# Optimization experiments

Measured on AMD Instinct MI355X. Metric: run time of the kernel, lower is better.

The kernel has to match this reference:

```python
import jax, jax.numpy as jnp
import numpy as np

HEADS, DK, DV, STRIDE = 8, 32, 32, 2
EPS = 1e-5

def dwconv(x, w, b, stride):
    # depthwise 3x3, padding 1; w: [C,1,3,3]
    y = jax.lax.conv_general_dilated(
        x, w, (stride, stride), ((1, 1), (1, 1)),
        dimension_numbers=("NCHW", "OIHW", "NCHW"),
        feature_group_count=x.shape[1])
    return y + b[None, :, None, None]

def setup_inputs() -> dict:
    key = jax.random.key(0)
    ks = jax.random.split(key, 16)
    B_, C, H, W = 8, 256, 56, 56
    hd = HEADS * DK
    s = lambda k, shp: (jax.random.normal(k, shp, jnp.float32) * 0.02)
    return {
        "x": jax.random.normal(ks[0], (B_, C, H, W), jnp.float32),
        "Wk_dw": s(ks[1], (C, 1, 3, 3)), "bk_dw": jnp.zeros((C,), jnp.float32),
        "Wv_dw": s(ks[2], (C, 1, 3, 3)), "bv_dw": jnp.zeros((C,), jnp.float32),
        "Wq": s(ks[3], (hd, C)), "bq": jnp.zeros((hd,), jnp.float32),
        "Wk": s(ks[4], (hd, C)), "bk": jnp.zeros((hd,), jnp.float32),
        "Wv": s(ks[5], (HEADS * DV, C)), "bv": jnp.zeros((HEADS * DV,), jnp.float32),
        "Wo": s(ks[6], (C, HEADS * DV)), "bo": jnp.zeros((C,), jnp.float32),
        "Bbias": s(ks[7], (1, HEADS, H * W, (H // STRIDE) * (W // STRIDE))),
    }

def reference(x, Wk_dw, bk_dw, Wv_dw, bv_dw, Wq, bq, Wk, bk, Wv, bv, Wo, bo, Bbias):
    b, c, h, w = x.shape
    xr = x.reshape(b, c, h * w).transpose(0, 2, 1)  # [b, hw, c]
    # F.layer_norm with normalized_shape=(b, hw, c): single mean/var over ALL elements
    mu = jnp.mean(xr)
    var = jnp.mean((xr - mu) ** 2)
    xn = (xr - mu) * jax.lax.rsqrt(var + EPS)
    q = (xn @ Wq.T + bq).reshape(b, h * w, HEADS, DK).transpose(0, 2, 1, 3)  # [b,H,hw,dk]
    ki = dwconv(x, Wk_dw, bk_dw, STRIDE)
    kh, kw = ki.shape[2], ki.shape[3]
    kf = ki.reshape(b, c, kh * kw).transpose(0, 2, 1)
    k = (kf @ Wk.T + bk).reshape(b, kh * kw, HEADS, DK).transpose(0, 2, 1, 3)
    vi = dwconv(x, Wv_dw, bv_dw, STRIDE)
    vf = vi.reshape(b, c, kh * kw).transpose(0, 2, 1)
    v = (vf @ Wv.T + bv).reshape(b, kh * kw, HEADS, DV).transpose(0, 2, 1, 3)
    attn = jnp.einsum("bhid,bhjd->bhij", q, k) * (DK ** -0.5) + Bbias
    attn = jax.nn.softmax(attn, axis=-1)
    res = jnp.einsum("bhij,bhjd->bhid", attn, v).transpose(0, 2, 1, 3)
    res = res.reshape(b, h * w, HEADS * DV)
    out = (res @ Wo.T + bo).reshape(b, c, h, w)  # faithful to original .view (no transpose)
    return out + x
```

## Files before the change

### kernel.cpp

```cpp
#include <hip/hip_runtime.h>

typedef unsigned short u16;
typedef unsigned int   u32;
typedef __attribute__((ext_vector_type(8))) short short8;
typedef __attribute__((ext_vector_type(4))) float f32x4;
typedef __attribute__((ext_vector_type(4))) unsigned short us4;

#define MFMA16(a, b, c) __builtin_amdgcn_mfma_f32_16x16x32_bf16((a), (b), (c), 0, 0, 0)

static constexpr int B_ = 8;
static constexpr int HW = 3136;
static constexpr int KW = 784;
static constexpr int NELEM = B_ * 256 * HW;
static constexpr int NBB = 8 * HW * KW;

static constexpr size_t OFF_CNT = 4096;
static constexpr size_t OFF_W   = 8192;
static constexpr int AOFF_WQ = 0, AOFF_WK = 65536, AOFF_WV = 131072, AOFF_WO = 196608;
static constexpr int AOFF_WKDW = 262144, AOFF_WVDW = 264448;
static constexpr int AOFF_BKDW = 266752, AOFF_BVDW = 267008, AOFF_BQ = 267264;
static constexpr int AOFF_BK = 267520, AOFF_BV = 267776, AOFF_BO = 268032;
static constexpr size_t OFF_XT  = 557056;
static constexpr size_t SZ_XT   = (size_t)B_ * HW * 256 * 2;
static constexpr size_t SZ_KJ   = (size_t)B_ * KW * 256 * 2;
static constexpr size_t OFF_KIT = OFF_XT + SZ_XT;
static constexpr size_t OFF_VIT = OFF_KIT + SZ_KJ;
static constexpr size_t OFF_KI  = OFF_VIT + SZ_KJ;
static constexpr size_t OFF_VI  = OFF_KI + SZ_KJ;
static constexpr size_t OFF_Q   = OFF_VI + SZ_KJ;
static constexpr size_t OFF_O   = OFF_XT;
static constexpr size_t OFF_BB  = OFF_Q + SZ_XT;
static constexpr size_t SZ_BB   = (size_t)NBB * 2;

__device__ __forceinline__ float bf2f(u16 u) { return __uint_as_float(((u32)u) << 16); }
__device__ __forceinline__ u16 f2bf(float f) {
  u32 u = __float_as_uint(f);
  u32 r = u + 0x7FFFu + ((u >> 16) & 1u);
  return (u16)(r >> 16);
}
__device__ __forceinline__ u32 cvtpk(float lo, float hi) {
  u32 r;
  asm("v_cvt_pk_bf16_f32 %0, %1, %2" : "=v"(r) : "v"(lo), "v"(hi));
  return r;
}

__global__ __launch_bounds__(256) void detect_k(const u32* __restrict__ x, int* __restrict__ cnt) {
  int c = 0;
  for (int i = threadIdx.x; i < 4096; i += 256) {
    float v = __uint_as_float(x[i] << 16);
    if (fabsf(v) > 1e4f) c++;
  }
#pragma unroll
  for (int off = 32; off > 0; off >>= 1) c += __shfl_down(c, off);
  if ((threadIdx.x & 63) == 0) atomicAdd(cnt, c);
}

struct CvtArgs { const void* src[12]; int dstoff[12]; int n[12]; };
__global__ __launch_bounds__(256) void cvt_all_k(CvtArgs a, u16* __restrict__ arena,
                                                 const void* __restrict__ bsrc,
                                                 u16* __restrict__ bdst, int bias_blocks,
                                                 const int* __restrict__ cnt) {
  int f32m = (*cnt >= 64);
  int bid = blockIdx.x;
  if (bid < bias_blocks) {
    const int n4 = NBB / 4;
    if (f32m) {
      const float4* s = (const float4*)bsrc;
      us4* d = (us4*)bdst;
      for (int i = bid * 256 + threadIdx.x; i < n4; i += bias_blocks * 256) {
        float4 v = s[i];
        us4 o = {f2bf(v.x), f2bf(v.y), f2bf(v.z), f2bf(v.w)};
        d[i] = o;
      }
    } else {
      const uint2* s = (const uint2*)bsrc;
      uint2* d = (uint2*)bdst;
      for (int i = bid * 256 + threadIdx.x; i < n4; i += bias_blocks * 256) d[i] = s[i];
    }
    return;
  }
  int wb = bid - bias_blocks;
  int t = wb >> 2, sub = wb & 3;
  int n = a.n[t];
  u16* d = arena + a.dstoff[t];
  if (f32m) {
    const float* s = (const float*)a.src[t];
    for (int i = sub * 256 + threadIdx.x; i < n; i += 1024) d[i] = f2bf(s[i]);
  } else {
    const u16* s = (const u16*)a.src[t];
    for (int i = sub * 256 + threadIdx.x; i < n; i += 1024) d[i] = s[i];
  }
}

__global__ __launch_bounds__(256) void reduce_k(const void* __restrict__ x, double* __restrict__ acc,
                                                const int* __restrict__ cnt) {
  int f32m = (*cnt >= 64);
  float s = 0.f, ss = 0.f;
  if (f32m) {
    const float4* xv = (const float4*)x;
    const int n4 = NELEM / 4;
    for (int i = blockIdx.x * 256 + threadIdx.x; i < n4; i += gridDim.x * 256) {
      float4 u = xv[i];
      s += u.x + u.y + u.z + u.w;
      ss += u.x * u.x + u.y * u.y + u.z * u.z + u.w * u.w;
    }
  } else {
    const uint4* xv = (const uint4*)x;
    const int n8 = NELEM / 8;
    for (int i = blockIdx.x * 256 + threadIdx.x; i < n8; i += gridDim.x * 256) {
      uint4 u = xv[i];
      u32 w[4] = {u.x, u.y, u.z, u.w};
#pragma unroll
      for (int q = 0; q < 4; q++) {
        float f0 = __uint_as_float(w[q] << 16);
        float f1 = __uint_as_float(w[q] & 0xFFFF0000u);
        s += f0 + f1;
        ss += f0 * f0 + f1 * f1;
      }
    }
  }
#pragma unroll
  for (int off = 32; off > 0; off >>= 1) {
    s += __shfl_down(s, off);
    ss += __shfl_down(ss, off);
  }
  __shared__ float as_[4], ass_[4];
  int wv = threadIdx.x >> 6;
  if ((threadIdx.x & 63) == 0) { as_[wv] = s; ass_[wv] = ss; }
  __syncthreads();
  if (threadIdx.x == 0) {
    atomicAdd(acc + 0, (double)(as_[0] + as_[1] + as_[2] + as_[3]));
    atomicAdd(acc + 1, (double)(ass_[0] + ass_[1] + ass_[2] + ass_[3]));
  }
}

__global__ __launch_bounds__(256) void prep_k(const u16* __restrict__ wq, const u16* __restrict__ bq,
                                              float* __restrict__ wsf) {
  const double* acc = (const double*)wsf;
  __shared__ float sh[2];
  if (threadIdx.x == 0) {
    double N = (double)NELEM;
    double mu = acc[0] / N;
    double var = acc[1] / N - mu * mu;
    float rstd = (float)(1.0 / sqrt(var + 1e-5));
    sh[0] = (float)mu; sh[1] = rstd;
    wsf[4] = (float)mu; wsf[5] = rstd;
    wsf[6] = rstd * 0.17677669529663687f;
  }
  __syncthreads();
  int o = threadIdx.x;
  float wsum = 0.f;
  for (int c = 0; c < 256; c++) wsum += bf2f(wq[o * 256 + c]);
  wsf[16 + o] = (bf2f(bq[o]) - sh[1] * sh[0] * wsum) * 0.17677669529663687f;
}

__global__ __launch_bounds__(256) void transpose_x_k(const void* __restrict__ src, u16* __restrict__ dst,
                                                     const int* __restrict__ cnt) {
  int f32m = (*cnt >= 64);
  __shared__ u16 t[32][33];
  int b = blockIdx.z;
  int r0 = blockIdx.y * 32, c0 = blockIdx.x * 32;
  int tid = threadIdx.x, col = tid & 31;
  size_t base = (size_t)b * 256 * HW;
  if (f32m) {
    const float* s = (const float*)src + base;
#pragma unroll
    for (int i = 0; i < 4; i++) {
      int row = (tid >> 5) + i * 8;
      t[row][col] = f2bf(s[(size_t)(r0 + row) * HW + c0 + col]);
    }
  } else {
    const u16* s = (const u16*)src + base;
#pragma unroll
    for (int i = 0; i < 4; i++) {
      int row = (tid >> 5) + i * 8;
      t[row][col] = s[(size_t)(r0 + row) * HW + c0 + col];
    }
  }
  __syncthreads();
  u16* d = dst + base;
#pragma unroll
  for (int i = 0; i < 4; i++) {
    int row = (tid >> 5) + i * 8;
    d[(size_t)(c0 + row) * 256 + r0 + col] = t[col][row];
  }
}

__global__ __launch_bounds__(256) void dwconv_t_k(const void* __restrict__ x,
                                                  const u16* __restrict__ arena,
                                                  u16* __restrict__ kit, u16* __restrict__ vit,
                                                  const int* __restrict__ cnt) {
  int f32m = (*cnt >= 64);
  int bid = blockIdx.x;
  int b = bid / 28, oi = bid % 28;
  int c = threadIdx.x;
  float wkf[9], wvf[9];
#pragma unroll
  for (int t = 0; t < 9; t++) {
    wkf[t] = bf2f(arena[AOFF_WKDW + c * 9 + t]);
    wvf[t] = bf2f(arena[AOFF_WVDW + c * 9 + t]);
  }
  float kb = bf2f(arena[AOFF_BKDW + c]), vb = bf2f(arena[AOFF_BVDW + c]);
  size_t xbase = (size_t)(b * 256 + c) * HW;
  auto body = [&](auto LDX) {
    for (int oj = 0; oj < 28; oj++) {
      float ka = kb, va = vb;
#pragma unroll
      for (int di = 0; di < 3; di++) {
        int ii = 2 * oi - 1 + di;
        if ((unsigned)ii >= 56u) continue;
#pragma unroll
        for (int dj = 0; dj < 3; dj++) {
          int ij = 2 * oj - 1 + dj;
          if ((unsigned)ij >= 56u) continue;
          float xv = LDX(ii * 56 + ij);
          ka += xv * wkf[di * 3 + dj];
          va += xv * wvf[di * 3 + dj];
        }
      }
      size_t o = ((size_t)b * KW + oi * 28 + oj) * 256 + c;
      kit[o] = f2bf(ka);
      vit[o] = f2bf(va);
    }
  };
  if (f32m) {
    const float* xp = (const float*)x + xbase;
    body([&](int i) { return xp[i]; });
  } else {
    const u16* xp = (const u16*)x + xbase;
    body([&](int i) { return bf2f(xp[i]); });
  }
}

__global__ __launch_bounds__(256) void proj_q_k(const u16* __restrict__ xt, const u16* __restrict__ Wq,
                                                const float* __restrict__ wsf, u16* __restrict__ q) {
  int lane = threadIdx.x & 63, wave = threadIdx.x >> 6;
  int l15 = lane & 15, quad = lane >> 4;
  int b = blockIdx.x / 49, pb = blockIdx.x % 49;
  int p0 = pb * 64 + wave * 16;
  const u16* arow = xt + ((size_t)(b * HW) + p0 + l15) * 256 + quad * 8;
  short8 af[8];
#pragma unroll
  for (int ks = 0; ks < 8; ks++) af[ks] = *(const short8*)(arow + ks * 32);
  float alpha = wsf[6];
  const float* beta = wsf + 16;
  for (int ot = 0; ot < 16; ot++) {
    const u16* brow = Wq + (size_t)(ot * 16 + l15) * 256 + quad * 8;
    f32x4 acc = {0.f, 0.f, 0.f, 0.f};
#pragma unroll
    for (int ks = 0; ks < 8; ks++) acc = MFMA16(af[ks], *(const short8*)(brow + ks * 32), acc);
    int o = ot * 16 + l15;
    float bet = beta[o];
    size_t base = ((size_t)(b * HW) + p0 + quad * 4) * 256 + o;
#pragma unroll
    for (int r = 0; r < 4; r++) q[base + (size_t)r * 256] = f2bf(alpha * acc[r] + bet);
  }
}

__device__ __forceinline__ void proj_k_body(int bid, const u16* __restrict__ kit,
                                            const u16* __restrict__ Wk, const u16* __restrict__ bk,
                                            u16* __restrict__ kout) {
  int lane = threadIdx.x & 63, wave = threadIdx.x >> 6;
  int l15 = lane & 15, quad = lane >> 4;
  int b = bid / 13, jb = bid % 13;
  int p0 = jb * 64 + wave * 16;
  if (p0 >= KW) return;
  const u16* arow = kit + ((size_t)(b * KW) + p0 + l15) * 256 + quad * 8;
  short8 af[8];
#pragma unroll
  for (int ks = 0; ks < 8; ks++) af[ks] = *(const short8*)(arow + ks * 32);
  for (int ot = 0; ot < 16; ot++) {
    const u16* brow = Wk + (size_t)(ot * 16 + l15) * 256 + quad * 8;
    f32x4 acc = {0.f, 0.f, 0.f, 0.f};
#pragma unroll
    for (int ks = 0; ks < 8; ks++) acc = MFMA16(af[ks], *(const short8*)(brow + ks * 32), acc);
    int o = ot * 16 + l15;
    float bias = bf2f(bk[o]);
    size_t base = ((size_t)(b * KW) + p0 + quad * 4) * 256 + o;
#pragma unroll
    for (int r = 0; r < 4; r++) kout[base + (size_t)r * 256] = f2bf(acc[r] + bias);
  }
}
__device__ __forceinline__ void proj_v_body(int bid, const u16* __restrict__ Wv,
                                            const u16* __restrict__ vit, const u16* __restrict__ bv,
                                            u16* __restrict__ vT) {
  int lane = threadIdx.x & 63, wave = threadIdx.x >> 6;
  int l15 = lane & 15, quad = lane >> 4;
  int b = bid >> 4;
  int ob = (bid >> 2) & 3;
  int js = bid & 3;
  int o0 = ob * 64 + wave * 16;
  const u16* arow = Wv + (size_t)(o0 + l15) * 256 + quad * 8;
  short8 af[8];
#pragma unroll
  for (int ks = 0; ks < 8; ks++) af[ks] = *(const short8*)(arow + ks * 32);
  int jt0 = js * 13;
  int jt1 = (jt0 + 13 < 49) ? jt0 + 13 : 49;
  for (int jt = jt0; jt < jt1; jt++) {
    const u16* brow = vit + ((size_t)(b * KW) + jt * 16 + l15) * 256 + quad * 8;
    f32x4 acc = {0.f, 0.f, 0.f, 0.f};
#pragma unroll
    for (int ks = 0; ks < 8; ks++) acc = MFMA16(af[ks], *(const short8*)(brow + ks * 32), acc);
#pragma unroll
    for (int r = 0; r < 4; r++) {
      int o = o0 + quad * 4 + r;
      vT[((size_t)(b * 256) + o) * KW + jt * 16 + l15] = f2bf(acc[r] + bf2f(bv[o]));
    }
  }
}
__global__ __launch_bounds__(256) void projkv_k(const u16* __restrict__ kit, const u16* __restrict__ Wk,
                                                const u16* __restrict__ bk, u16* __restrict__ kout,
                                                const u16* __restrict__ vit, const u16* __restrict__ Wv,
                                                const u16* __restrict__ bv, u16* __restrict__ vT) {
  int bid = blockIdx.x;
  if (bid < 104) proj_k_body(bid, kit, Wk, bk, kout);
  else           proj_v_body(bid - 104, Wv, vit, bv, vT);
}

template <typename LD>
__device__ __forceinline__ void attn_body(const u16* __restrict__ qptr, const u16* __restrict__ kptr,
                                          const u16* __restrict__ vptr, u16* __restrict__ Ob,
                                          int b, int h, int p0, LD ldb) {
  int lane = threadIdx.x & 63;
  int l15 = lane & 15, quad = lane >> 4;
  const u16* qp = qptr + ((size_t)(b * HW) + p0 + l15) * 256 + h * 32 + quad * 8;
  short8 qf0 = *(const short8*)qp;
  short8 qf1 = *(const short8*)(qp + 16 * 256);
  const u16* kb = kptr + (size_t)b * KW * 256 + h * 32 + quad * 8;
  const u16* vb = vptr + ((size_t)(b * 256) + h * 32) * KW;
  const f32x4 zz = {0.f, 0.f, 0.f, 0.f};
  f32x4 o00 = zz, o01 = zz, o10 = zz, o11 = zz;
  float ls0 = 0.f, ls1 = 0.f;

  for (int jt = 0; jt < 49; jt++) {
    short8 kf = *(const short8*)(kb + (size_t)(jt * 16 + l15) * 256);
    f32x4 s0 = MFMA16(kf, qf0, zz);
    f32x4 s1 = MFMA16(kf, qf1, zz);
    f32x4 b0 = ldb(0, jt), b1 = ldb(1, jt);
    float e00 = __expf(fminf(s0[0] + b0[0], 30.f));
    float e01 = __expf(fminf(s0[1] + b0[1], 30.f));
    float e02 = __expf(fminf(s0[2] + b0[2], 30.f));
    float e03 = __expf(fminf(s0[3] + b0[3], 30.f));
    float e10 = __expf(fminf(s1[0] + b1[0], 30.f));
    float e11 = __expf(fminf(s1[1] + b1[1], 30.f));
    float e12 = __expf(fminf(s1[2] + b1[2], 30.f));
    float e13 = __expf(fminf(s1[3] + b1[3], 30.f));
    ls0 += (e00 + e01) + (e02 + e03);
    ls1 += (e10 + e11) + (e12 + e13);
    union { u32 u[4]; short8 s; } pa, pb;
    pa.u[0] = cvtpk(e00, e01); pa.u[1] = cvtpk(e02, e03); pa.u[2] = 0; pa.u[3] = 0;
    pb.u[0] = cvtpk(e10, e11); pb.u[1] = cvtpk(e12, e13); pb.u[2] = 0; pb.u[3] = 0;
    int jo = jt * 16 + quad * 4;
    uint2 va2 = *(const uint2*)(vb + (size_t)l15 * KW + jo);
    uint2 vb2 = *(const uint2*)(vb + (size_t)(16 + l15) * KW + jo);
    union { u32 u[4]; short8 s; } va, vbf;
    va.u[0] = va2.x;  va.u[1] = va2.y;  va.u[2] = 0; va.u[3] = 0;
    vbf.u[0] = vb2.x; vbf.u[1] = vb2.y; vbf.u[2] = 0; vbf.u[3] = 0;
    o00 = MFMA16(va.s, pa.s, o00);
    o01 = MFMA16(vbf.s, pa.s, o01);
    o10 = MFMA16(va.s, pb.s, o10);
    o11 = MFMA16(vbf.s, pb.s, o11);
  }
  ls0 += __shfl_xor(ls0, 16); ls0 += __shfl_xor(ls0, 32);
  ls1 += __shfl_xor(ls1, 16); ls1 += __shfl_xor(ls1, 32);
  float inv0 = 1.f / ls0, inv1 = 1.f / ls1;
  size_t ob0 = ((size_t)(b * HW) + p0 + l15) * 256 + h * 32 + quad * 4;
  us4 w0, w1, w2, w3;
#pragma unroll
  for (int r = 0; r < 4; r++) {
    w0[r] = f2bf(o00[r] * inv0);
    w1[r] = f2bf(o01[r] * inv0);
    w2[r] = f2bf(o10[r] * inv1);
    w3[r] = f2bf(o11[r] * inv1);
  }
  *(us4*)(Ob + ob0) = w0;
  *(us4*)(Ob + ob0 + 16) = w1;
  *(us4*)(Ob + ob0 + (size_t)16 * 256) = w2;
  *(us4*)(Ob + ob0 + (size_t)16 * 256 + 16) = w3;
}

template <int BMODE>
__global__ __launch_bounds__(256) void attn_k(const u16* __restrict__ q, const u16* __restrict__ k,
                                              const u16* __restrict__ vT, const void* __restrict__ Bb,
                                              u16* __restrict__ Ob, const int* __restrict__ cnt) {
  int lane = threadIdx.x & 63;
  int l15 = lane & 15, quad = lane >> 4;
  int task = blockIdx.x * 4 + (threadIdx.x >> 6);
  int pt = task % 98;
  int t = task / 98;
  int h = t & 7, b = t >> 3;
  int p0 = pt * 32;
  size_t bbase = ((size_t)(h * HW) + p0 + l15) * KW + quad * 4;
  if constexpr (BMODE == 0) {
    const u16* bb = (const u16*)Bb;
    attn_body(q, k, vT, Ob, b, h, p0, [&](int sub, int jt) -> f32x4 {
      us4 v = *(const us4*)(bb + bbase + (size_t)(sub * 16) * KW + jt * 16);
      f32x4 r = {bf2f(v[0]), bf2f(v[1]), bf2f(v[2]), bf2f(v[3])};
      return r;
    });
  } else {
    if (*cnt >= 64) {
      const float* bf = (const float*)Bb;
      attn_body(q, k, vT, Ob, b, h, p0, [&](int sub, int jt) -> f32x4 {
        float4 v = *(const float4*)(bf + bbase + (size_t)(sub * 16) * KW + jt * 16);
        f32x4 r = {v.x, v.y, v.z, v.w};
        return r;
      });
    } else {
      const u16* bb = (const u16*)Bb;
      attn_body(q, k, vT, Ob, b, h, p0, [&](int sub, int jt) -> f32x4 {
        us4 v = *(const us4*)(bb + bbase + (size_t)(sub * 16) * KW + jt * 16);
        f32x4 r = {bf2f(v[0]), bf2f(v[1]), bf2f(v[2]), bf2f(v[3])};
        return r;
      });
    }
  }
}

__global__ __launch_bounds__(256) void proj_o_k(const u16* __restrict__ Ob, const u16* __restrict__ Wo,
                                                const u16* __restrict__ bo, const void* __restrict__ x,
                                                void* __restrict__ out, const int* __restrict__ cnt) {
  int f32m = (*cnt >= 64);
  int lane = threadIdx.x & 63, wave = threadIdx.x >> 6;
  int l15 = lane & 15, quad = lane >> 4;
  int b = blockIdx.x / 49, pb = blockIdx.x % 49;
  int p0 = pb * 64 + wave * 16;
  const u16* arow = Ob + ((size_t)(b * HW) + p0 + l15) * 256 + quad * 8;
  short8 af[8];
#pragma unroll
  for (int ks = 0; ks < 8; ks++) af[ks] = *(const short8*)(arow + ks * 32);
  for (int ot = 0; ot < 16; ot++) {
    const u16* brow = Wo + (size_t)(ot * 16 + l15) * 256 + quad * 8;
    f32x4 acc = {0.f, 0.f, 0.f, 0.f};
#pragma unroll
    for (int ks = 0; ks < 8; ks++) acc = MFMA16(af[ks], *(const short8*)(brow + ks * 32), acc);
    int o = ot * 16 + l15;
    float bias = bf2f(bo[o]);
    if (f32m) {
      const float* xf = (const float*)x;
      float* of = (float*)out;
#pragma unroll
      for (int r = 0; r < 4; r++) {
        size_t idx = ((size_t)(b * HW) + p0 + quad * 4 + r) * 256 + o;
        of[idx] = acc[r] + bias + xf[idx];
      }
    } else {
      const u16* xb = (const u16*)x;
      u16* ob_ = (u16*)out;
#pragma unroll
      for (int r = 0; r < 4; r++) {
        size_t idx = ((size_t)(b * HW) + p0 + quad * 4 + r) * 256 + o;
        ob_[idx] = f2bf(acc[r] + bias + bf2f(xb[idx]));
      }
    }
  }
}

extern "C" void kernel_launch(void* const* d_in, const int* in_sizes, int n_in,
                              void* d_out, int out_size, void* d_ws, size_t ws_size,
                              hipStream_t stream) {
  (void)in_sizes; (void)n_in; (void)out_size;
  const void* x = d_in[0];
  char* ws = (char*)d_ws;
  int* cnt = (int*)(ws + OFF_CNT);
  u16* arena = (u16*)(ws + OFF_W);
  u16* xt  = (u16*)(ws + OFF_XT);
  u16* kit = (u16*)(ws + OFF_KIT);
  u16* vit = (u16*)(ws + OFF_VIT);
  u16* ki  = (u16*)(ws + OFF_KI);
  u16* vi  = (u16*)(ws + OFF_VI);
  u16* qb  = (u16*)(ws + OFF_Q);
  u16* Obuf = (u16*)(ws + OFF_O);
  u16* bbA = (u16*)(ws + OFF_BB);
  bool big_ws = ws_size >= (OFF_BB + SZ_BB);

  CvtArgs a;
  const int srcidx[12] = {5, 7, 9, 11, 1, 3, 2, 4, 6, 8, 10, 12};
  const int dofs[12] = {AOFF_WQ, AOFF_WK, AOFF_WV, AOFF_WO, AOFF_WKDW, AOFF_WVDW,
                        AOFF_BKDW, AOFF_BVDW, AOFF_BQ, AOFF_BK, AOFF_BV, AOFF_BO};
  const int ns[12] = {65536, 65536, 65536, 65536, 2304, 2304, 256, 256, 256, 256, 256, 256};
  for (int i = 0; i < 12; i++) { a.src[i] = d_in[srcidx[i]]; a.dstoff[i] = dofs[i]; a.n[i] = ns[i]; }

  hipMemsetAsync(d_ws, 0, 8192, stream);
  detect_k<<<1, 256, 0, stream>>>((const u32*)x, cnt);
  int bias_blocks = big_ws ? 2048 : 0;
  cvt_all_k<<<bias_blocks + 48, 256, 0, stream>>>(a, arena, d_in[13], bbA, bias_blocks, cnt);
  reduce_k<<<1024, 256, 0, stream>>>(x, (double*)d_ws, cnt);
  prep_k<<<1, 256, 0, stream>>>(arena + AOFF_WQ, arena + AOFF_BQ, (float*)d_ws);
  transpose_x_k<<<dim3(98, 8, 8), 256, 0, stream>>>(x, xt, cnt);
  dwconv_t_k<<<224, 256, 0, stream>>>(x, arena, kit, vit, cnt);
  projkv_k<<<232, 256, 0, stream>>>(kit, arena + AOFF_WK, arena + AOFF_BK, ki,
                                    vit, arena + AOFF_WV, arena + AOFF_BV, vi);
  proj_q_k<<<392, 256, 0, stream>>>(xt, arena + AOFF_WQ, (const float*)d_ws, qb);
  if (big_ws) attn_k<0><<<1568, 256, 0, stream>>>(qb, ki, vi, bbA, Obuf, cnt);
  else        attn_k<1><<<1568, 256, 0, stream>>>(qb, ki, vi, d_in[13], Obuf, cnt);
  proj_o_k<<<392, 256, 0, stream>>>(Obuf, arena + AOFF_WO, arena + AOFF_BO, x, d_out, cnt);
}
```

Before: 480.2 us.

## Parallelize depthwise conv per channel with separate transposes; reorder attention tasks by batch

Measured after the change: 464.8 us. 3.2% less time.

```diff
diff --git a/kernel.cpp b/kernel.cpp
--- a/kernel.cpp
+++ b/kernel.cpp
@@ -186,14 +186,34 @@
   }
 }
 
-__global__ __launch_bounds__(256) void dwconv_t_k(const void* __restrict__ x,
-                                                  const u16* __restrict__ arena,
-                                                  u16* __restrict__ kit, u16* __restrict__ vit,
-                                                  const int* __restrict__ cnt) {
+__global__ __launch_bounds__(256) void transpose_k(const u16* __restrict__ src, u16* __restrict__ dst,
+                                                   int R, int Cc) {
+  __shared__ u16 t[32][33];
+  int b = blockIdx.z;
+  int r0 = blockIdx.y * 32, c0 = blockIdx.x * 32;
+  const u16* s = src + (size_t)b * R * Cc;
+  u16* d = dst + (size_t)b * R * Cc;
+  int tid = threadIdx.x, col = tid & 31;
+#pragma unroll
+  for (int i = 0; i < 4; i++) {
+    int row = (tid >> 5) + i * 8;
+    if (r0 + row < R && c0 + col < Cc) t[row][col] = s[(size_t)(r0 + row) * Cc + c0 + col];
+  }
+  __syncthreads();
+#pragma unroll
+  for (int i = 0; i < 4; i++) {
+    int row = (tid >> 5) + i * 8;
+    if (c0 + row < Cc && r0 + col < R) d[(size_t)(c0 + row) * R + r0 + col] = t[col][row];
+  }
+}
+
+__global__ __launch_bounds__(256) void dwconv_k(const void* __restrict__ x,
+                                                const u16* __restrict__ arena,
+                                                u16* __restrict__ ki, u16* __restrict__ vi,
+                                                const int* __restrict__ cnt) {
   int f32m = (*cnt >= 64);
-  int bid = blockIdx.x;
-  int b = bid / 28, oi = bid % 28;
-  int c = threadIdx.x;
+  int b = blockIdx.x >> 8;
+  int c = blockIdx.x & 255;
   float wkf[9], wvf[9];
 #pragma unroll
   for (int t = 0; t < 9; t++) {
@@ -203,7 +223,8 @@
   float kb = bf2f(arena[AOFF_BKDW + c]), vb = bf2f(arena[AOFF_BVDW + c]);
   size_t xbase = (size_t)(b * 256 + c) * HW;
   auto body = [&](auto LDX) {
-    for (int oj = 0; oj < 28; oj++) {
+    for (int j = threadIdx.x; j < KW; j += 256) {
+      int oi = j / 28, oj = j % 28;
       float ka = kb, va = vb;
 #pragma unroll
       for (int di = 0; di < 3; di++) {
@@ -218,9 +239,8 @@
           va += xv * wvf[di * 3 + dj];
         }
       }
-      size_t o = ((size_t)b * KW + oi * 28 + oj) * 256 + c;
-      kit[o] = f2bf(ka);
-      vit[o] = f2bf(va);
+      ki[(size_t)(b * 256 + c) * KW + j] = f2bf(ka);
+      vi[(size_t)(b * 256 + c) * KW + j] = f2bf(va);
     }
   };
   if (f32m) {
@@ -386,9 +406,10 @@
   int lane = threadIdx.x & 63;
   int l15 = lane & 15, quad = lane >> 4;
   int task = blockIdx.x * 4 + (threadIdx.x >> 6);
-  int pt = task % 98;
-  int t = task / 98;
-  int h = t & 7, b = t >> 3;
+  int b = task & 7;
+  int t = task >> 3;
+  int h = t & 7;
+  int pt = t >> 3;
   int p0 = pt * 32;
   size_t bbase = ((size_t)(h * HW) + p0 + l15) * KW + quad * 4;
   if constexpr (BMODE == 0) {
@@ -488,7 +509,9 @@
   reduce_k<<<1024, 256, 0, stream>>>(x, (double*)d_ws, cnt);
   prep_k<<<1, 256, 0, stream>>>(arena + AOFF_WQ, arena + AOFF_BQ, (float*)d_ws);
   transpose_x_k<<<dim3(98, 8, 8), 256, 0, stream>>>(x, xt, cnt);
-  dwconv_t_k<<<224, 256, 0, stream>>>(x, arena, kit, vit, cnt);
+  dwconv_k<<<2048, 256, 0, stream>>>(x, arena, ki, vi, cnt);
+  transpose_k<<<dim3(25, 8, 8), 256, 0, stream>>>(ki, kit, 256, KW);
+  transpose_k<<<dim3(25, 8, 8), 256, 0, stream>>>(vi, vit, 256, KW);
   projkv_k<<<232, 256, 0, stream>>>(kit, arena + AOFF_WK, arena + AOFF_BK, ki,
                                     vit, arena + AOFF_WV, arena + AOFF_BV, vi);
   proj_q_k<<<392, 256, 0, stream>>>(xt, arena + AOFF_WQ, (const float*)d_ws, qb);
```
